# Performance work log

Measured on AMD Instinct MI355X. Metric: run time of the kernel, lower is better.

## Reference

```python
import jax, jax.numpy as jnp
import numpy as np

RES = 300          # grid resolution per axis
NC_D = 16          # density_n_comp
NC_A = 48          # app_n_comp
APP_DIM = 27       # app_dim
N = 500000         # number of ray samples

MAT_MODE = [[0, 1], [0, 2], [1, 2]]
VEC_MODE = [2, 1, 0]


def setup_inputs() -> dict:
    key = jax.random.key(0)
    k0, k1, k2, k3 = jax.random.split(key, 4)
    xyz_sampled = jax.random.uniform(k0, (N, 3), minval=-1.0, maxval=1.0, dtype=jnp.float32)
    plane_coef = 0.1 * jax.random.normal(k1, (3, NC_A + NC_D, RES, RES), dtype=jnp.float32)
    line_coef = 0.1 * jax.random.normal(k2, (3, NC_A + NC_D, RES, 1), dtype=jnp.float32)
    basis_W = jax.random.normal(k3, (APP_DIM, 3 * NC_A), dtype=jnp.float32) / np.sqrt(3 * NC_A)
    return {"xyz_sampled": xyz_sampled, "plane_coef": plane_coef,
            "line_coef": line_coef, "basis_W": basis_W}


def _grid_sample(img, x, y):
    """Bilinear grid_sample, align_corners=True, zeros padding.
    img: (C, H, W); x, y: (N,) normalized coords in [-1, 1] (x -> W, y -> H).
    Returns (C, N)."""
    C, H, W = img.shape
    ix = (x + 1.0) * 0.5 * (W - 1)
    iy = (y + 1.0) * 0.5 * (H - 1)
    x0f = jnp.floor(ix)
    y0f = jnp.floor(iy)
    wx = ix - x0f   # weight for x0+1
    wy = iy - y0f   # weight for y0+1
    x0 = x0f.astype(jnp.int32)
    y0 = y0f.astype(jnp.int32)
    out = jnp.zeros((C, x.shape[0]), img.dtype)
    for dx, wxc in ((0, 1.0 - wx), (1, wx)):
        for dy, wyc in ((0, 1.0 - wy), (1, wy)):
            xi = x0 + dx
            yi = y0 + dy
            valid = (xi >= 0) & (xi < W) & (yi >= 0) & (yi < H)
            xic = jnp.clip(xi, 0, W - 1)
            yic = jnp.clip(yi, 0, H - 1)
            w = jnp.where(valid, wxc * wyc, 0.0)
            out = out + img[:, yic, xic] * w
    return out


def reference(xyz_sampled, plane_coef, line_coef, basis_W):
    zeros = jnp.zeros((xyz_sampled.shape[0],), xyz_sampled.dtype)
    pf, lf = [], []
    for i in range(3):
        m0, m1 = MAT_MODE[i]
        # plane: grid = (x=xyz[m0] -> W, y=xyz[m1] -> H)
        pf.append(_grid_sample(plane_coef[i], xyz_sampled[:, m0], xyz_sampled[:, m1]))
        # line: grid = (x=0 -> W(=1), y=xyz[vecMode] -> H) => 1D interp along H
        lf.append(_grid_sample(line_coef[i], zeros, xyz_sampled[:, VEC_MODE[i]]))
    pf = jnp.stack(pf)  # (3, NC_A+NC_D, N)
    lf = jnp.stack(lf)  # (3, NC_A+NC_D, N)
    # compute_densityfeature: last density_n_comp channels, multiply and sum-reduce
    sigma_feature = jnp.sum(pf[:, NC_A:] * lf[:, NC_A:], axis=(0, 1))  # (N,)
    # compute_appfeature: first app_n_comp channels, multiply then basis projection
    app_feats = (pf[:, :NC_A] * lf[:, :NC_A]).reshape(3 * NC_A, -1)    # (3*NC_A, N)
    app_features = app_feats.T @ basis_W.T                              # (N, APP_DIM)
    return sigma_feature, app_features
```

## Files before the change

### kernel.cpp

```cpp
#include <hip/hip_runtime.h>
#include <hip/hip_bf16.h>

#define RES 300
#define NPLANE (RES * RES)
#define NC_A 48
#define APP_DIM 27
#define KDIM 144
#define KS 168

#define PT_TILES 352
#define NPBLK (3 * PT_TILES)
#define LSS 268

__device__ __forceinline__ float bf_lo(unsigned int u) { return __uint_as_float(u << 16); }
__device__ __forceinline__ float bf_hi(unsigned int u) { return __uint_as_float(u & 0xffff0000u); }

__global__ __launch_bounds__(256) void prep(
    const float* __restrict__ plane, const float* __restrict__ line,
    const float* __restrict__ W,
    __hip_bfloat16* __restrict__ Tp, unsigned int* __restrict__ TlP,
    __hip_bfloat16* __restrict__ Wg) {
  __shared__ unsigned short ls[64 * LSS];
  const int blk = blockIdx.x;
  const int tid = threadIdx.x;

  if (blk < NPBLK) {
    const int i    = blk / PT_TILES;
    const int p0   = (blk % PT_TILES) * 256;
    const int l    = tid & 63;
    const int w    = tid >> 6;
    const int pl   = p0 + 4 * l;
    const bool pok = (pl + 3) < NPLANE;
    #pragma unroll
    for (int r = 0; r < 16; ++r) {
      int c = w * 16 + r;
      float4 v = make_float4(0.f, 0.f, 0.f, 0.f);
      if (pok) v = *(const float4*)&plane[(size_t)(i * 64 + c) * NPLANE + pl];
      __hip_bfloat162 h0, h1;
      h0.x = __float2bfloat16(v.x); h0.y = __float2bfloat16(v.y);
      h1.x = __float2bfloat16(v.z); h1.y = __float2bfloat16(v.w);
      uint2 u;
      u.x = *(unsigned int*)&h0;
      u.y = *(unsigned int*)&h1;
      *(uint2*)&ls[c * LSS + 4 * l] = u;
    }
    __syncthreads();
    const size_t obase = ((size_t)i * NPLANE + p0) * 64;
    const int plim = min(256, NPLANE - p0);
    #pragma unroll
    for (int r = 0; r < 8; ++r) {
      int flat4 = r * 256 + tid;
      int p  = flat4 >> 3;
      int c0 = (flat4 & 7) * 8;
      if (p < plim) {
        unsigned int x0 = (unsigned int)ls[(c0 + 0) * LSS + p] |
                          ((unsigned int)ls[(c0 + 1) * LSS + p] << 16);
        unsigned int x1 = (unsigned int)ls[(c0 + 2) * LSS + p] |
                          ((unsigned int)ls[(c0 + 3) * LSS + p] << 16);
        unsigned int x2 = (unsigned int)ls[(c0 + 4) * LSS + p] |
                          ((unsigned int)ls[(c0 + 5) * LSS + p] << 16);
        unsigned int x3 = (unsigned int)ls[(c0 + 6) * LSS + p] |
                          ((unsigned int)ls[(c0 + 7) * LSS + p] << 16);
        uint4 o = {x0, x1, x2, x3};
        *(uint4*)&Tp[obase + (size_t)p * 64 + c0] = o;
      }
    }
  } else if (blk < NPBLK + 15) {
    unsigned int* ltile = (unsigned int*)ls;
    const int b  = blk - NPBLK;
    const int i  = b / 5;
    const int y0 = (b % 5) * 64;
    const int yl = tid & 63;
    const int cq = tid >> 6;
    #pragma unroll
    for (int k = 0; k < 16; ++k) {
      int c = cq * 16 + k;
      int y = y0 + yl;
      float a = 0.f, bv = 0.f;
      if (y < RES) {
        const float* row = line + (i * 64 + c) * RES;
        a  = row[y];
        bv = row[min(y + 1, RES - 1)];
      }
      __hip_bfloat162 h;
      h.x = __float2bfloat16(a);
      h.y = __float2bfloat16(bv);
      ltile[yl * 65 + c] = *(unsigned int*)&h;
    }
    __syncthreads();
    #pragma unroll
    for (int k = 0; k < 16; ++k) {
      int ylc = k * 4 + cq;
      int c   = tid & 63;
      int y   = y0 + ylc;
      if (y < RES) TlP[((size_t)i * RES + y) * 64 + c] = ltile[ylc * 65 + c];
    }
  } else {
    for (int idx = tid; idx < 2 * 5 * 64 * 8; idx += 256) {
      int j    = idx & 7;
      int lane = (idx >> 3) & 63;
      int kt   = (idx >> 9) % 5;
      int tile = idx / (5 * 64 * 8);
      int n = tile * 16 + (lane & 15);
      int k = kt * 32 + (lane >> 4) * 8 + j;
      float v = (n < APP_DIM && k < KDIM) ? W[n * KDIM + k] : 0.f;
      Wg[idx] = __float2bfloat16(v);
    }
  }
}

typedef __attribute__((ext_vector_type(8))) short short8;
typedef __attribute__((ext_vector_type(4))) float f32x4;

__global__ __launch_bounds__(256, 6) void tensorf_main(
    const float* __restrict__ xyz, const unsigned int* __restrict__ TpU,
    const unsigned int* __restrict__ TlP, const __hip_bfloat16* __restrict__ Wg,
    float* __restrict__ out, int n_total) {
  __shared__ __hip_bfloat16 prod[64 * KS];
  __shared__ float cw[64 * 18];

  const int tid  = threadIdx.x;
  const int lane = tid & 63;
  const int wave = tid >> 6;
  const int n0   = blockIdx.x * 64;

  for (int j = tid; j < 64 * 12; j += 256) {
    int s = j / 12, kk = (j % 12) * 2;
    *(unsigned int*)&prod[s * KS + KDIM + kk] = 0u;
  }

  if (tid < 64) {
    int n = min(n0 + tid, n_total - 1);
    float crd[3] = {xyz[3 * n], xyz[3 * n + 1], xyz[3 * n + 2]};
    const int m0s[3] = {0, 0, 1}, m1s[3] = {1, 2, 2}, vms[3] = {2, 1, 0};
    float* c = &cw[tid * 18];
    #pragma unroll
    for (int i = 0; i < 3; ++i) {
      float ix = fminf(fmaxf((crd[m0s[i]] + 1.f) * 149.5f, 0.f), 299.f);
      float iy = fminf(fmaxf((crd[m1s[i]] + 1.f) * 149.5f, 0.f), 299.f);
      float ly = fminf(fmaxf((crd[vms[i]] + 1.f) * 149.5f, 0.f), 299.f);
      float x0f = fminf(floorf(ix), 298.f);
      float y0f = fminf(floorf(iy), 298.f);
      float l0f = fminf(floorf(ly), 298.f);
      float wx = ix - x0f, wy = iy - y0f, lwy = ly - l0f;
      int cell = i * NPLANE + (int)y0f * RES + (int)x0f;
      int lidx = i * RES + (int)l0f;
      c[i * 6 + 0] = __int_as_float(cell | (lidx << 19));
      c[i * 6 + 1] = (1.f - wx) * (1.f - wy);
      c[i * 6 + 2] = wx * (1.f - wy);
      c[i * 6 + 3] = (1.f - wx) * wy;
      c[i * 6 + 4] = wx * wy;
      c[i * 6 + 5] = lwy;
    }
  }
  __syncthreads();

  const int cl   = lane & 31;
  const int half = lane >> 5;
  const int c2   = cl * 2;
  #pragma unroll 2
  for (int it = 0; it < 8; ++it) {
    int s = wave * 16 + it * 2 + half;
    const float* cp = &cw[s * 18];

    unsigned int u00[3], u01[3], u10[3], u11[3];
    uint2 ul[3];
    float wgt[3][5];
    #pragma unroll
    for (int i = 0; i < 3; ++i) {
      float2 q0 = *(const float2*)&cp[i * 6];
      float2 q1 = *(const float2*)&cp[i * 6 + 2];
      float2 q2 = *(const float2*)&cp[i * 6 + 4];
      int pk   = __float_as_int(q0.x);
      int cell = pk & 0x7FFFF;
      int lidx = pk >> 19;
      int bidx = cell * 32 + cl;
      u00[i] = TpU[bidx];
      u01[i] = TpU[bidx + 32];
      u10[i] = TpU[bidx + RES * 32];
      u11[i] = TpU[bidx + RES * 32 + 32];
      ul[i]  = *(const uint2*)&TlP[(lidx << 6) + c2];
      wgt[i][0] = q0.y; wgt[i][1] = q1.x; wgt[i][2] = q1.y;
      wgt[i][3] = q2.x; wgt[i][4] = q2.y;
    }

    float dsum = 0.f;
    #pragma unroll
    for (int i = 0; i < 3; ++i) {
      float pf_l = wgt[i][0] * bf_lo(u00[i]) + wgt[i][1] * bf_lo(u01[i]) +
                   wgt[i][2] * bf_lo(u10[i]) + wgt[i][3] * bf_lo(u11[i]);
      float pf_h = wgt[i][0] * bf_hi(u00[i]) + wgt[i][1] * bf_hi(u01[i]) +
                   wgt[i][2] * bf_hi(u10[i]) + wgt[i][3] * bf_hi(u11[i]);
      float lal = bf_lo(ul[i].x), lbl = bf_hi(ul[i].x);
      float lah = bf_lo(ul[i].y), lbh = bf_hi(ul[i].y);
      float lf_l = lal + wgt[i][4] * (lbl - lal);
      float lf_h = lah + wgt[i][4] * (lbh - lah);
      float prl = pf_l * lf_l, prh = pf_h * lf_h;
      if (cl < 24) {
        __hip_bfloat162 h;
        h.x = __float2bfloat16(prl);
        h.y = __float2bfloat16(prh);
        *(unsigned int*)&prod[s * KS + i * NC_A + c2] = *(unsigned int*)&h;
      } else {
        dsum += prl + prh;
      }
    }
    dsum += __shfl_xor(dsum, 1);
    dsum += __shfl_xor(dsum, 2);
    dsum += __shfl_xor(dsum, 4);
    int n = n0 + s;
    if (cl == 24 && n < n_total) out[n] = dsum;
  }
  __syncthreads();

  const int srow = lane & 15, quad = lane >> 4;
  f32x4 acc0 = {0.f, 0.f, 0.f, 0.f}, acc1 = {0.f, 0.f, 0.f, 0.f};
  const short* prodS = (const short*)prod;
  const short* WgS   = (const short*)Wg;
  const int arow = (wave * 16 + srow) * KS;
  #pragma unroll
  for (int kt = 0; kt < 5; ++kt) {
    short8 a  = *(const short8*)&prodS[arow + kt * 32 + quad * 8];
    short8 b0 = *(const short8*)&WgS[(kt * 64 + lane) * 8];
    short8 b1 = *(const short8*)&WgS[((5 + kt) * 64 + lane) * 8];
    acc0 = __builtin_amdgcn_mfma_f32_16x16x32_bf16(a, b0, acc0, 0, 0, 0);
    acc1 = __builtin_amdgcn_mfma_f32_16x16x32_bf16(a, b1, acc1, 0, 0, 0);
  }
  float* outApp = out + n_total;
  #pragma unroll
  for (int r = 0; r < 4; ++r) {
    int n = n0 + wave * 16 + quad * 4 + r;
    if (n < n_total) {
      outApp[(size_t)n * APP_DIM + srow] = acc0[r];
      if (srow < APP_DIM - 16)
        outApp[(size_t)n * APP_DIM + 16 + srow] = acc1[r];
    }
  }
}

extern "C" void kernel_launch(void* const* d_in, const int* in_sizes, int n_in,
                              void* d_out, int out_size, void* d_ws, size_t ws_size,
                              hipStream_t stream) {
  const float* xyz   = (const float*)d_in[0];
  const float* plane = (const float*)d_in[1];
  const float* line  = (const float*)d_in[2];
  const float* W     = (const float*)d_in[3];
  float* out = (float*)d_out;
  const int N = in_sizes[0] / 3;

  char* ws = (char*)d_ws;
  __hip_bfloat16* Tp  = (__hip_bfloat16*)ws;
  unsigned int*   TlP = (unsigned int*)(ws + 34560000);
  __hip_bfloat16* Wg  = (__hip_bfloat16*)(ws + 34560000 + 230400);

  prep<<<NPBLK + 16, 256, 0, stream>>>(plane, line, W, Tp, TlP, Wg);
  tensorf_main<<<(N + 63) / 64, 256, 0, stream>>>(
      xyz, (const unsigned int*)Tp, TlP, Wg, out, N);
}
```

Before: 228.1 us.

## Store x-neighbor pairs interleaved in plane table to halve gather loads

The prep kernel can now write a plane table that stores each texel together with its x+1 neighbour for each channel pair. The main kernel then fetches a bilinear row with one 8-byte load per row instead of two 4-byte loads. Packed float2 math is also used for the interpolation. The cost is a plane table twice the size, which means more prep write traffic and a larger cache footprint. The path is chosen at runtime from the workspace size and falls back to the old layout when the workspace is too small.

```diff
diff --git a/kernel.cpp b/kernel.cpp
--- a/kernel.cpp
+++ b/kernel.cpp
@@ -12,13 +12,24 @@
 #define NPBLK (3 * PT_TILES)
 #define LSS 268
 
+typedef __attribute__((ext_vector_type(2))) float f32x2;
+typedef __attribute__((ext_vector_type(4))) float f32x4;
+typedef __attribute__((ext_vector_type(8))) short short8;
+
 __device__ __forceinline__ float bf_lo(unsigned int u) { return __uint_as_float(u << 16); }
 __device__ __forceinline__ float bf_hi(unsigned int u) { return __uint_as_float(u & 0xffff0000u); }
+__device__ __forceinline__ f32x2 bfp(unsigned int u) { f32x2 r = {bf_lo(u), bf_hi(u)}; return r; }
+__device__ __forceinline__ unsigned int packbf2(f32x2 v) {
+  __hip_bfloat162 h;
+  h.x = __float2bfloat16(v.x);
+  h.y = __float2bfloat16(v.y);
+  return *(unsigned int*)&h;
+}
 
 __global__ __launch_bounds__(256) void prep(
     const float* __restrict__ plane, const float* __restrict__ line,
-    const float* __restrict__ W,
-    __hip_bfloat16* __restrict__ Tp, unsigned int* __restrict__ TlP,
+    const float* __restrict__ W, int xpair,
+    unsigned int* __restrict__ Tp, unsigned int* __restrict__ TlP,
     __hip_bfloat16* __restrict__ Wg) {
   __shared__ unsigned short ls[64 * LSS];
   const int blk = blockIdx.x;
@@ -44,25 +55,57 @@
       u.y = *(unsigned int*)&h1;
       *(uint2*)&ls[c * LSS + 4 * l] = u;
     }
+    if (tid < 64) {
+      float v = 0.f;
+      int pe = p0 + 256;
+      if (pe < NPLANE) v = plane[(size_t)(i * 64 + tid) * NPLANE + pe];
+      __hip_bfloat16 hb = __float2bfloat16(v);
+      ls[tid * LSS + 256] = *(unsigned short*)&hb;
+    }
     __syncthreads();
-    const size_t obase = ((size_t)i * NPLANE + p0) * 64;
     const int plim = min(256, NPLANE - p0);
-    #pragma unroll
-    for (int r = 0; r < 8; ++r) {
-      int flat4 = r * 256 + tid;
-      int p  = flat4 >> 3;
-      int c0 = (flat4 & 7) * 8;
-      if (p < plim) {
-        unsigned int x0 = (unsigned int)ls[(c0 + 0) * LSS + p] |
-                          ((unsigned int)ls[(c0 + 1) * LSS + p] << 16);
-        unsigned int x1 = (unsigned int)ls[(c0 + 2) * LSS + p] |
-                          ((unsigned int)ls[(c0 + 3) * LSS + p] << 16);
-        unsigned int x2 = (unsigned int)ls[(c0 + 4) * LSS + p] |
-                          ((unsigned int)ls[(c0 + 5) * LSS + p] << 16);
-        unsigned int x3 = (unsigned int)ls[(c0 + 6) * LSS + p] |
-                          ((unsigned int)ls[(c0 + 7) * LSS + p] << 16);
-        uint4 o = {x0, x1, x2, x3};
-        *(uint4*)&Tp[obase + (size_t)p * 64 + c0] = o;
+    if (xpair) {
+      const size_t ob = ((size_t)i * NPLANE + p0) * 64;
+      #pragma unroll
+      for (int r = 0; r < 16; ++r) {
+        int idx = r * 256 + tid;
+        int p = idx >> 4, q = idx & 15;
+        if (p < plim) {
+          int pg = p0 + p;
+          int x  = pg - (pg / RES) * RES;
+          int pn = (x == RES - 1) ? p : p + 1;
+          int c0 = q * 4;
+          unsigned int e0 = (unsigned int)ls[(c0 + 0) * LSS + p]  |
+                            ((unsigned int)ls[(c0 + 1) * LSS + p]  << 16);
+          unsigned int e1 = (unsigned int)ls[(c0 + 0) * LSS + pn] |
+                            ((unsigned int)ls[(c0 + 1) * LSS + pn] << 16);
+          unsigned int e2 = (unsigned int)ls[(c0 + 2) * LSS + p]  |
+                            ((unsigned int)ls[(c0 + 3) * LSS + p]  << 16);
+          unsigned int e3 = (unsigned int)ls[(c0 + 2) * LSS + pn] |
+                            ((unsigned int)ls[(c0 + 3) * LSS + pn] << 16);
+          uint4 o = {e0, e1, e2, e3};
+          *(uint4*)&Tp[ob + (size_t)p * 64 + q * 4] = o;
+        }
+      }
+    } else {
+      const size_t ob = ((size_t)i * NPLANE + p0) * 32;
+      #pragma unroll
+      for (int r = 0; r < 8; ++r) {
+        int flat4 = r * 256 + tid;
+        int p  = flat4 >> 3;
+        int c0 = (flat4 & 7) * 8;
+        if (p < plim) {
+          unsigned int x0 = (unsigned int)ls[(c0 + 0) * LSS + p] |
+                            ((unsigned int)ls[(c0 + 1) * LSS + p] << 16);
+          unsigned int x1 = (unsigned int)ls[(c0 + 2) * LSS + p] |
+                            ((unsigned int)ls[(c0 + 3) * LSS + p] << 16);
+          unsigned int x2 = (unsigned int)ls[(c0 + 4) * LSS + p] |
+                            ((unsigned int)ls[(c0 + 5) * LSS + p] << 16);
+          unsigned int x3 = (unsigned int)ls[(c0 + 6) * LSS + p] |
+                            ((unsigned int)ls[(c0 + 7) * LSS + p] << 16);
+          uint4 o = {x0, x1, x2, x3};
+          *(uint4*)&Tp[ob + (size_t)p * 32 + c0 / 2] = o;
+        }
       }
     }
   } else if (blk < NPBLK + 15) {
@@ -109,9 +152,7 @@
   }
 }
 
-typedef __attribute__((ext_vector_type(8))) short short8;
-typedef __attribute__((ext_vector_type(4))) float f32x4;
-
+template <bool XP>
 __global__ __launch_bounds__(256, 6) void tensorf_main(
     const float* __restrict__ xyz, const unsigned int* __restrict__ TpU,
     const unsigned int* __restrict__ TlP, const __hip_bfloat16* __restrict__ Wg,
@@ -163,53 +204,90 @@
     int s = wave * 16 + it * 2 + half;
     const float* cp = &cw[s * 18];
 
-    unsigned int u00[3], u01[3], u10[3], u11[3];
-    uint2 ul[3];
-    float wgt[3][5];
-    #pragma unroll
-    for (int i = 0; i < 3; ++i) {
-      float2 q0 = *(const float2*)&cp[i * 6];
-      float2 q1 = *(const float2*)&cp[i * 6 + 2];
-      float2 q2 = *(const float2*)&cp[i * 6 + 4];
-      int pk   = __float_as_int(q0.x);
-      int cell = pk & 0x7FFFF;
-      int lidx = pk >> 19;
-      int bidx = cell * 32 + cl;
-      u00[i] = TpU[bidx];
-      u01[i] = TpU[bidx + 32];
-      u10[i] = TpU[bidx + RES * 32];
-      u11[i] = TpU[bidx + RES * 32 + 32];
-      ul[i]  = *(const uint2*)&TlP[(lidx << 6) + c2];
-      wgt[i][0] = q0.y; wgt[i][1] = q1.x; wgt[i][2] = q1.y;
-      wgt[i][3] = q2.x; wgt[i][4] = q2.y;
-    }
-
-    float dsum = 0.f;
-    #pragma unroll
-    for (int i = 0; i < 3; ++i) {
-      float pf_l = wgt[i][0] * bf_lo(u00[i]) + wgt[i][1] * bf_lo(u01[i]) +
-                   wgt[i][2] * bf_lo(u10[i]) + wgt[i][3] * bf_lo(u11[i]);
-      float pf_h = wgt[i][0] * bf_hi(u00[i]) + wgt[i][1] * bf_hi(u01[i]) +
-                   wgt[i][2] * bf_hi(u10[i]) + wgt[i][3] * bf_hi(u11[i]);
-      float lal = bf_lo(ul[i].x), lbl = bf_hi(ul[i].x);
-      float lah = bf_lo(ul[i].y), lbh = bf_hi(ul[i].y);
-      float lf_l = lal + wgt[i][4] * (lbl - lal);
-      float lf_h = lah + wgt[i][4] * (lbh - lah);
-      float prl = pf_l * lf_l, prh = pf_h * lf_h;
-      if (cl < 24) {
-        __hip_bfloat162 h;
-        h.x = __float2bfloat16(prl);
-        h.y = __float2bfloat16(prh);
-        *(unsigned int*)&prod[s * KS + i * NC_A + c2] = *(unsigned int*)&h;
-      } else {
-        dsum += prl + prh;
-      }
-    }
-    dsum += __shfl_xor(dsum, 1);
-    dsum += __shfl_xor(dsum, 2);
-    dsum += __shfl_xor(dsum, 4);
-    int n = n0 + s;
-    if (cl == 24 && n < n_total) out[n] = dsum;
+    if (XP) {
+      uint2 r0[3], r1[3], ul[3];
+      float wgt[3][5];
+      #pragma unroll
+      for (int i = 0; i < 3; ++i) {
+        float2 q0 = *(const float2*)&cp[i * 6];
+        float2 q1 = *(const float2*)&cp[i * 6 + 2];
+        float2 q2 = *(const float2*)&cp[i * 6 + 4];
+        int pk   = __float_as_int(q0.x);
+        int cell = pk & 0x7FFFF;
+        int lidx = pk >> 19;
+        const uint2* Tp2 = (const uint2*)TpU;
+        int b2 = cell * 32 + cl;
+        r0[i] = Tp2[b2];
+        r1[i] = Tp2[b2 + RES * 32];
+        ul[i] = *(const uint2*)&TlP[(lidx << 6) + c2];
+        wgt[i][0] = q0.y; wgt[i][1] = q1.x; wgt[i][2] = q1.y;
+        wgt[i][3] = q2.x; wgt[i][4] = q2.y;
+      }
+      f32x2 dsum2 = {0.f, 0.f};
+      #pragma unroll
+      for (int i = 0; i < 3; ++i) {
+        f32x2 a0 = bfp(r0[i].x), b0 = bfp(r0[i].y);
+        f32x2 a1 = bfp(r1[i].x), b1 = bfp(r1[i].y);
+        f32x2 pf = a0 * wgt[i][0] + b0 * wgt[i][1] +
+                   a1 * wgt[i][2] + b1 * wgt[i][3];
+        f32x2 la = {bf_lo(ul[i].x), bf_lo(ul[i].y)};
+        f32x2 lb = {bf_hi(ul[i].x), bf_hi(ul[i].y)};
+        f32x2 pr = pf * (la + wgt[i][4] * (lb - la));
+        if (cl < 24) *(unsigned int*)&prod[s * KS + i * NC_A + c2] = packbf2(pr);
+        else         dsum2 += pr;
+      }
+      float dsum = dsum2.x + dsum2.y;
+      dsum += __shfl_xor(dsum, 1);
+      dsum += __shfl_xor(dsum, 2);
+      dsum += __shfl_xor(dsum, 4);
+      int n = n0 + s;
+      if (cl == 24 && n < n_total) out[n] = dsum;
+    } else {
+      unsigned int u00[3], u01[3], u10[3], u11[3];
+      uint2 ul[3];
+      float wgt[3][5];
+      #pragma unroll
+      for (int i = 0; i < 3; ++i) {
+        float2 q0 = *(const float2*)&cp[i * 6];
+        float2 q1 = *(const float2*)&cp[i * 6 + 2];
+        float2 q2 = *(const float2*)&cp[i * 6 + 4];
+        int pk   = __float_as_int(q0.x);
+        int cell = pk & 0x7FFFF;
+        int lidx = pk >> 19;
+        int bidx = cell * 32 + cl;
+        u00[i] = TpU[bidx];
+        u01[i] = TpU[bidx + 32];
+        u10[i] = TpU[bidx + RES * 32];
+        u11[i] = TpU[bidx + RES * 32 + 32];
+        ul[i]  = *(const uint2*)&TlP[(lidx << 6) + c2];
+        wgt[i][0] = q0.y; wgt[i][1] = q1.x; wgt[i][2] = q1.y;
+        wgt[i][3] = q2.x; wgt[i][4] = q2.y;
+      }
+      float dsum = 0.f;
+      #pragma unroll
+      for (int i = 0; i < 3; ++i) {
+        float pf_l = wgt[i][0] * bf_lo(u00[i]) + wgt[i][1] * bf_lo(u01[i]) +
+                     wgt[i][2] * bf_lo(u10[i]) + wgt[i][3] * bf_lo(u11[i]);
+        float pf_h = wgt[i][0] * bf_hi(u00[i]) + wgt[i][1] * bf_hi(u01[i]) +
+                     wgt[i][2] * bf_hi(u10[i]) + wgt[i][3] * bf_hi(u11[i]);
+        float lal = bf_lo(ul[i].x), lbl = bf_hi(ul[i].x);
+        float lah = bf_lo(ul[i].y), lbh = bf_hi(ul[i].y);
+        float lf_l = lal + wgt[i][4] * (lbl - lal);
+        float lf_h = lah + wgt[i][4] * (lbh - lah);
+        float prl = pf_l * lf_l, prh = pf_h * lf_h;
+        if (cl < 24) {
+          f32x2 pr = {prl, prh};
+          *(unsigned int*)&prod[s * KS + i * NC_A + c2] = packbf2(pr);
+        } else {
+          dsum += prl + prh;
+        }
+      }
+      dsum += __shfl_xor(dsum, 1);
+      dsum += __shfl_xor(dsum, 2);
+      dsum += __shfl_xor(dsum, 4);
+      int n = n0 + s;
+      if (cl == 24 && n < n_total) out[n] = dsum;
+    }
   }
   __syncthreads();
 
@@ -248,12 +326,19 @@
   float* out = (float*)d_out;
   const int N = in_sizes[0] / 3;
 
+  const size_t tp_xp    = (size_t)3 * NPLANE * 256;
+  const size_t tp_plain = (size_t)3 * NPLANE * 128;
+  const bool   xp = ws_size >= tp_xp + 230400 + 10240;
+  const size_t tp_bytes = xp ? tp_xp : tp_plain;
+
   char* ws = (char*)d_ws;
-  __hip_bfloat16* Tp  = (__hip_bfloat16*)ws;
-  unsigned int*   TlP = (unsigned int*)(ws + 34560000);
-  __hip_bfloat16* Wg  = (__hip_bfloat16*)(ws + 34560000 + 230400);
-
-  prep<<<NPBLK + 16, 256, 0, stream>>>(plane, line, W, Tp, TlP, Wg);
-  tensorf_main<<<(N + 63) / 64, 256, 0, stream>>>(
-      xyz, (const unsigned int*)Tp, TlP, Wg, out, N);
+  unsigned int*   Tp  = (unsigned int*)ws;
+  unsigned int*   TlP = (unsigned int*)(ws + tp_bytes);
+  __hip_bfloat16* Wg  = (__hip_bfloat16*)(ws + tp_bytes + 230400);
+
+  prep<<<NPBLK + 16, 256, 0, stream>>>(plane, line, W, xp ? 1 : 0, Tp, TlP, Wg);
+  if (xp)
+    tensorf_main<true><<<(N + 63) / 64, 256, 0, stream>>>(xyz, Tp, TlP, Wg, out, N);
+  else
+    tensorf_main<false><<<(N + 63) / 64, 256, 0, stream>>>(xyz, Tp, TlP, Wg, out, N);
 }
```

Result: slower. 241.2 us (+5.7%).

## Sort samples into Morton-ordered spatial buckets before gathering plane features

Applied to the files above, without the earlier changes.

Adds a counting sort (histogram, scan, scatter) that reorders ray samples by a 16^3 Morton bucket, so neighbouring samples in a block gather nearby plane cells and cache locality improves. The main kernel reads the permuted float4 points, carries each point's original index through shared memory, and scatters both outputs back to the original positions. The cost is four extra small kernel launches, atomics, an extra pass over xyz, and scattered output writes. It falls back to the unsorted path when the workspace is too small.

```diff
diff --git a/kernel.cpp b/kernel.cpp
--- a/kernel.cpp
+++ b/kernel.cpp
@@ -7,18 +7,42 @@
 #define APP_DIM 27
 #define KDIM 144
 #define KS 168
+#define CWS 20
 
 #define PT_TILES 352
 #define NPBLK (3 * PT_TILES)
 #define LSS 268
+#define NBUCK 4096
+
+typedef __attribute__((ext_vector_type(2))) float f32x2;
+typedef __attribute__((ext_vector_type(4))) float f32x4;
+typedef __attribute__((ext_vector_type(8))) short short8;
 
 __device__ __forceinline__ float bf_lo(unsigned int u) { return __uint_as_float(u << 16); }
 __device__ __forceinline__ float bf_hi(unsigned int u) { return __uint_as_float(u & 0xffff0000u); }
+__device__ __forceinline__ unsigned int packbf2(float a, float b) {
+  __hip_bfloat162 h;
+  h.x = __float2bfloat16(a);
+  h.y = __float2bfloat16(b);
+  return *(unsigned int*)&h;
+}
+
+__device__ __forceinline__ int bucket_of(float x, float y, float z) {
+  int bx = min(max((int)((x + 1.f) * 8.f), 0), 15);
+  int by = min(max((int)((y + 1.f) * 8.f), 0), 15);
+  int bz = min(max((int)((z + 1.f) * 8.f), 0), 15);
+  int m = 0;
+  #pragma unroll
+  for (int i = 0; i < 4; ++i)
+    m |= (((bx >> i) & 1) << (3 * i)) | (((by >> i) & 1) << (3 * i + 1)) |
+         (((bz >> i) & 1) << (3 * i + 2));
+  return m;
+}
 
 __global__ __launch_bounds__(256) void prep(
     const float* __restrict__ plane, const float* __restrict__ line,
     const float* __restrict__ W,
-    __hip_bfloat16* __restrict__ Tp, unsigned int* __restrict__ TlP,
+    unsigned int* __restrict__ Tp, unsigned int* __restrict__ TlP,
     __hip_bfloat16* __restrict__ Wg) {
   __shared__ unsigned short ls[64 * LSS];
   const int blk = blockIdx.x;
@@ -36,16 +60,13 @@
       int c = w * 16 + r;
       float4 v = make_float4(0.f, 0.f, 0.f, 0.f);
       if (pok) v = *(const float4*)&plane[(size_t)(i * 64 + c) * NPLANE + pl];
-      __hip_bfloat162 h0, h1;
-      h0.x = __float2bfloat16(v.x); h0.y = __float2bfloat16(v.y);
-      h1.x = __float2bfloat16(v.z); h1.y = __float2bfloat16(v.w);
       uint2 u;
-      u.x = *(unsigned int*)&h0;
-      u.y = *(unsigned int*)&h1;
+      u.x = packbf2(v.x, v.y);
+      u.y = packbf2(v.z, v.w);
       *(uint2*)&ls[c * LSS + 4 * l] = u;
     }
     __syncthreads();
-    const size_t obase = ((size_t)i * NPLANE + p0) * 64;
+    const size_t ob = ((size_t)i * NPLANE + p0) * 32;
     const int plim = min(256, NPLANE - p0);
     #pragma unroll
     for (int r = 0; r < 8; ++r) {
@@ -62,7 +83,7 @@
         unsigned int x3 = (unsigned int)ls[(c0 + 6) * LSS + p] |
                           ((unsigned int)ls[(c0 + 7) * LSS + p] << 16);
         uint4 o = {x0, x1, x2, x3};
-        *(uint4*)&Tp[obase + (size_t)p * 64 + c0] = o;
+        *(uint4*)&Tp[ob + (size_t)p * 32 + c0 / 2] = o;
       }
     }
   } else if (blk < NPBLK + 15) {
@@ -82,10 +103,7 @@
         a  = row[y];
         bv = row[min(y + 1, RES - 1)];
       }
-      __hip_bfloat162 h;
-      h.x = __float2bfloat16(a);
-      h.y = __float2bfloat16(bv);
-      ltile[yl * 65 + c] = *(unsigned int*)&h;
+      ltile[yl * 65 + c] = packbf2(a, bv);
     }
     __syncthreads();
     #pragma unroll
@@ -109,15 +127,64 @@
   }
 }
 
-typedef __attribute__((ext_vector_type(8))) short short8;
-typedef __attribute__((ext_vector_type(4))) float f32x4;
-
+__global__ __launch_bounds__(256) void k_zero(int* __restrict__ hist) {
+  int i = blockIdx.x * 256 + threadIdx.x;
+  if (i < NBUCK) hist[i] = 0;
+}
+
+__global__ __launch_bounds__(256) void k_hist(
+    const float* __restrict__ xyz, int* __restrict__ hist, int n_total) {
+  int n = blockIdx.x * 256 + threadIdx.x;
+  if (n < n_total) {
+    int b = bucket_of(xyz[3 * n], xyz[3 * n + 1], xyz[3 * n + 2]);
+    atomicAdd(&hist[b], 1);
+  }
+}
+
+__global__ __launch_bounds__(1024) void k_scan(int* __restrict__ hist) {
+  __shared__ int sd[1024];
+  const int tid = threadIdx.x;
+  int carry = 0;
+  for (int ch = 0; ch < NBUCK / 1024; ++ch) {
+    int i = ch * 1024 + tid;
+    int v = hist[i];
+    sd[tid] = v;
+    __syncthreads();
+    #pragma unroll
+    for (int off = 1; off < 1024; off <<= 1) {
+      int t = (tid >= off) ? sd[tid - off] : 0;
+      __syncthreads();
+      sd[tid] += t;
+      __syncthreads();
+    }
+    int incl = sd[tid];
+    int total = sd[1023];
+    hist[i] = incl - v + carry;
+    carry += total;
+    __syncthreads();
+  }
+}
+
+__global__ __launch_bounds__(256) void k_scatter(
+    const float* __restrict__ xyz, int* __restrict__ hist,
+    float4* __restrict__ xyzP, int n_total) {
+  int n = blockIdx.x * 256 + threadIdx.x;
+  if (n < n_total) {
+    float x = xyz[3 * n], y = xyz[3 * n + 1], z = xyz[3 * n + 2];
+    int b = bucket_of(x, y, z);
+    int pos = atomicAdd(&hist[b], 1);
+    xyzP[pos] = make_float4(x, y, z, __int_as_float(n));
+  }
+}
+
+template <bool SORTED>
 __global__ __launch_bounds__(256, 6) void tensorf_main(
-    const float* __restrict__ xyz, const unsigned int* __restrict__ TpU,
-    const unsigned int* __restrict__ TlP, const __hip_bfloat16* __restrict__ Wg,
+    const float* __restrict__ xyz, const float4* __restrict__ xyzP,
+    const unsigned int* __restrict__ TpU, const unsigned int* __restrict__ TlP,
+    const __hip_bfloat16* __restrict__ Wg,
     float* __restrict__ out, int n_total) {
   __shared__ __hip_bfloat16 prod[64 * KS];
-  __shared__ float cw[64 * 18];
+  __shared__ float cw[64 * CWS];
 
   const int tid  = threadIdx.x;
   const int lane = tid & 63;
@@ -131,9 +198,18 @@
 
   if (tid < 64) {
     int n = min(n0 + tid, n_total - 1);
-    float crd[3] = {xyz[3 * n], xyz[3 * n + 1], xyz[3 * n + 2]};
+    float crd[3];
+    int orig;
+    if (SORTED) {
+      float4 q = xyzP[n];
+      crd[0] = q.x; crd[1] = q.y; crd[2] = q.z;
+      orig = __float_as_int(q.w);
+    } else {
+      crd[0] = xyz[3 * n]; crd[1] = xyz[3 * n + 1]; crd[2] = xyz[3 * n + 2];
+      orig = n;
+    }
     const int m0s[3] = {0, 0, 1}, m1s[3] = {1, 2, 2}, vms[3] = {2, 1, 0};
-    float* c = &cw[tid * 18];
+    float* c = &cw[tid * CWS];
     #pragma unroll
     for (int i = 0; i < 3; ++i) {
       float ix = fminf(fmaxf((crd[m0s[i]] + 1.f) * 149.5f, 0.f), 299.f);
@@ -152,6 +228,7 @@
       c[i * 6 + 4] = wx * wy;
       c[i * 6 + 5] = lwy;
     }
+    c[18] = __int_as_float(orig);
   }
   __syncthreads();
 
@@ -161,7 +238,7 @@
   #pragma unroll 2
   for (int it = 0; it < 8; ++it) {
     int s = wave * 16 + it * 2 + half;
-    const float* cp = &cw[s * 18];
+    const float* cp = &cw[s * CWS];
 
     unsigned int u00[3], u01[3], u10[3], u11[3];
     uint2 ul[3];
@@ -197,10 +274,7 @@
       float lf_h = lah + wgt[i][4] * (lbh - lah);
       float prl = pf_l * lf_l, prh = pf_h * lf_h;
       if (cl < 24) {
-        __hip_bfloat162 h;
-        h.x = __float2bfloat16(prl);
-        h.y = __float2bfloat16(prh);
-        *(unsigned int*)&prod[s * KS + i * NC_A + c2] = *(unsigned int*)&h;
+        *(unsigned int*)&prod[s * KS + i * NC_A + c2] = packbf2(prl, prh);
       } else {
         dsum += prl + prh;
       }
@@ -208,8 +282,10 @@
     dsum += __shfl_xor(dsum, 1);
     dsum += __shfl_xor(dsum, 2);
     dsum += __shfl_xor(dsum, 4);
-    int n = n0 + s;
-    if (cl == 24 && n < n_total) out[n] = dsum;
+    if (cl == 24) {
+      int orig = __float_as_int(cw[s * CWS + 18]);
+      out[orig] = dsum;
+    }
   }
   __syncthreads();
 
@@ -229,12 +305,11 @@
   float* outApp = out + n_total;
   #pragma unroll
   for (int r = 0; r < 4; ++r) {
-    int n = n0 + wave * 16 + quad * 4 + r;
-    if (n < n_total) {
-      outApp[(size_t)n * APP_DIM + srow] = acc0[r];
-      if (srow < APP_DIM - 16)
-        outApp[(size_t)n * APP_DIM + 16 + srow] = acc1[r];
-    }
+    int sr = wave * 16 + quad * 4 + r;
+    int orig = __float_as_int(cw[sr * CWS + 18]);
+    outApp[(size_t)orig * APP_DIM + srow] = acc0[r];
+    if (srow < APP_DIM - 16)
+      outApp[(size_t)orig * APP_DIM + 16 + srow] = acc1[r];
   }
 }
 
@@ -248,12 +323,32 @@
   float* out = (float*)d_out;
   const int N = in_sizes[0] / 3;
 
+  const size_t tp_b   = (size_t)3 * NPLANE * 128;
+  const size_t tl_b   = 230400;
+  const size_t wg_b   = 10240 + 5888;
+  const size_t hist_b = (size_t)NBUCK * 4;
+  const size_t xyzp_b = (size_t)N * 16;
+
   char* ws = (char*)d_ws;
-  __hip_bfloat16* Tp  = (__hip_bfloat16*)ws;
-  unsigned int*   TlP = (unsigned int*)(ws + 34560000);
-  __hip_bfloat16* Wg  = (__hip_bfloat16*)(ws + 34560000 + 230400);
+  unsigned int*   Tp   = (unsigned int*)ws;
+  unsigned int*   TlP  = (unsigned int*)(ws + tp_b);
+  __hip_bfloat16* Wg   = (__hip_bfloat16*)(ws + tp_b + tl_b);
+  int*            hist = (int*)(ws + tp_b + tl_b + wg_b);
+  float4*         xyzP = (float4*)(ws + tp_b + tl_b + wg_b + hist_b);
+
+  const bool sorted = ws_size >= tp_b + tl_b + wg_b + hist_b + xyzp_b;
+  const int nblk = (N + 255) / 256;
 
   prep<<<NPBLK + 16, 256, 0, stream>>>(plane, line, W, Tp, TlP, Wg);
-  tensorf_main<<<(N + 63) / 64, 256, 0, stream>>>(
-      xyz, (const unsigned int*)Tp, TlP, Wg, out, N);
-}
+  if (sorted) {
+    k_zero<<<(NBUCK + 255) / 256, 256, 0, stream>>>(hist);
+    k_hist<<<nblk, 256, 0, stream>>>(xyz, hist, N);
+    k_scan<<<1, 1024, 0, stream>>>(hist);
+    k_scatter<<<nblk, 256, 0, stream>>>(xyz, hist, xyzP, N);
+    tensorf_main<true><<<(N + 63) / 64, 256, 0, stream>>>(
+        xyz, xyzP, Tp, TlP, Wg, out, N);
+  } else {
+    tensorf_main<false><<<(N + 63) / 64, 256, 0, stream>>>(
+        xyz, nullptr, Tp, TlP, Wg, out, N);
+  }
+}
```

Result: slower. 309.5 us (+35.7%).
